# Optimization experiments

Measured on AMD Instinct MI355X. Metric: run time of the kernel, lower is better.

Reference implementation:

```python
import jax, jax.numpy as jnp
import numpy as np

B, L, D = 2, 2048, 1024
DH = 64
NH = D // DH
EPS = 1e-5
NEG = -1e30


def rms_norm(x, w):
    # x: (..., dh); norm in fp32 like the torch module, then scale by weight
    xf = x.astype(jnp.float32)
    y = xf * jax.lax.rsqrt(jnp.mean(xf * xf, axis=-1, keepdims=True) + EPS)
    return y.astype(x.dtype) * w.astype(x.dtype)


def sdpa(q, k, v, m):
    # q:(b,h,lq,dh) k,v:(b,h,lk,dh) m:(lq,lk) bool
    scale = 1.0 / jnp.sqrt(jnp.asarray(DH, q.dtype))
    s = jnp.einsum('bhqd,bhkd->bhqk', q, k) * scale
    s = jnp.where(m[None, None], s, NEG)
    p = jax.nn.softmax(s, axis=-1)
    return jnp.einsum('bhqk,bhkd->bhqd', p, v)


def setup_inputs() -> dict:
    key = jax.random.key(0)
    k1, k2, k3 = jax.random.split(key, 3)
    x = jax.random.normal(k1, (B, L, D), dtype=jnp.float32)
    mask = jnp.tril(jnp.ones((L, L), dtype=bool))  # causal: no fully-masked rows
    w_qkv = jax.random.normal(k2, (3 * D, D), dtype=jnp.float32) * (1.0 / np.sqrt(D))
    w_fc = jax.random.normal(k3, (D, D), dtype=jnp.float32) * (1.0 / np.sqrt(D))
    q_norm_w = jnp.ones((DH,), dtype=jnp.float32)
    k_norm_w = jnp.ones((DH,), dtype=jnp.float32)
    return {"x": x, "mask": mask, "w_qkv": w_qkv, "w_fc": w_fc,
            "q_norm_w": q_norm_w, "k_norm_w": k_norm_w,
            "subset_attention_size": 1024}


def reference(x, mask, w_qkv, w_fc, q_norm_w, k_norm_w, subset_attention_size):
    b, l, d = x.shape
    qkv = jnp.einsum('bld,ed->ble', x, w_qkv)  # (b,l,3d)
    q, k, v = jnp.split(qkv, 3, axis=-1)

    def heads(t):
        return t.reshape(b, l, NH, DH).transpose(0, 2, 1, 3)  # (b,nh,l,dh)

    q, k, v = heads(q), heads(k), heads(v)
    q = rms_norm(q, q_norm_w)
    k = rms_norm(k, k_norm_w)

    S = subset_attention_size
    if S is not None and S < l:
        o1 = sdpa(q[:, :, :S], k[:, :, :S], v[:, :, :S], mask[:S, :S])
        o2 = sdpa(q[:, :, S:], k, v, mask[S:, :])
        o = jnp.concatenate([o1, o2], axis=2)
    else:
        o = sdpa(q, k, v, mask)
    o = o.transpose(0, 2, 1, 3).reshape(b, l, d)  # (b,l,d)
    return jnp.einsum('bld,ed->ble', o, w_fc)
```

## Files before the change

kernel.cpp:

```cpp
#include <hip/hip_runtime.h>

typedef __bf16 bf16x8 __attribute__((ext_vector_type(8)));
typedef __bf16 bf16x4 __attribute__((ext_vector_type(4)));
typedef float f32x4 __attribute__((ext_vector_type(4)));
typedef unsigned short u16;
typedef unsigned int u32;
typedef unsigned short u16x4 __attribute__((ext_vector_type(4)));
typedef unsigned short u16x8 __attribute__((ext_vector_type(8)));

#define AS1 __attribute__((address_space(1)))
#define AS3 __attribute__((address_space(3)))

__device__ __forceinline__ u16 f2bf(float f) {
  unsigned u = __builtin_bit_cast(unsigned, f);
  u += 0x7fffu + ((u >> 16) & 1u);
  return (u16)(u >> 16);
}

__global__ __launch_bounds__(256) void cvt_all(const float* __restrict__ x,
                                               const float* __restrict__ wq,
                                               const float* __restrict__ wf,
                                               u16* __restrict__ xb, u16* __restrict__ wqb,
                                               u16* __restrict__ wfb) {
  long i = ((long)blockIdx.x * 256 + threadIdx.x) * 4;
  const float* src;
  u16* dst;
  long off;
  if (i < 4194304L) {
    src = x; dst = xb; off = i;
  } else if (i < 7340032L) {
    src = wq; dst = wqb; off = i - 4194304L;
  } else {
    src = wf; dst = wfb; off = i - 7340032L;
  }
  float4 v = *reinterpret_cast<const float4*>(src + off);
  u16x4 o;
  o.x = f2bf(v.x); o.y = f2bf(v.y); o.z = f2bf(v.z); o.w = f2bf(v.w);
  *reinterpret_cast<u16x4*>(dst + off) = o;
}

__global__ __launch_bounds__(256, 2) void gemm_qkv(const u16* __restrict__ A,
                                                   const u16* __restrict__ W,
                                                   u16* __restrict__ C,
                                                   const float* __restrict__ qw,
                                                   const float* __restrict__ kw) {
  constexpr int N = 3072, K = 1024;
  __shared__ __align__(16) u16 As[128 * 32];
  __shared__ __align__(16) u16 Bs[128 * 32];
  const int tid = threadIdx.x;
  const int lane = tid & 63;
  const int wid = tid >> 6;
  const int wm = wid >> 1, wn = wid & 1;
  const int l16 = lane & 15, g4 = lane >> 4;
  const long bm = blockIdx.x, bn = blockIdx.y;

  const int srow = tid >> 2;
  const int scol = (tid & 3) * 8;
  const u16* aA0 = A + (bm * 128 + srow) * (long)K + scol;
  const u16* aA1 = aA0 + 64 * (long)K;
  const u16* aW0 = W + (bn * 128 + srow) * (long)K + scol;
  const u16* aW1 = aW0 + 64 * (long)K;

  f32x4 acc[4][4] = {};

  for (int kt = 0; kt < K; kt += 32) {
    __builtin_amdgcn_global_load_lds((AS1 void*)(aA0 + kt), (AS3 void*)(&As[tid * 8]), 16, 0, 0);
    __builtin_amdgcn_global_load_lds((AS1 void*)(aA1 + kt), (AS3 void*)(&As[2048 + tid * 8]), 16, 0, 0);
    __builtin_amdgcn_global_load_lds((AS1 void*)(aW0 + kt), (AS3 void*)(&Bs[tid * 8]), 16, 0, 0);
    __builtin_amdgcn_global_load_lds((AS1 void*)(aW1 + kt), (AS3 void*)(&Bs[2048 + tid * 8]), 16, 0, 0);
    __syncthreads();
    bf16x8 af[4], bfr[4];
#pragma unroll
    for (int m = 0; m < 4; ++m)
      af[m] = *reinterpret_cast<const bf16x8*>(&As[(wm * 64 + m * 16 + l16) * 32 + g4 * 8]);
#pragma unroll
    for (int n = 0; n < 4; ++n)
      bfr[n] = *reinterpret_cast<const bf16x8*>(&Bs[(wn * 64 + n * 16 + l16) * 32 + g4 * 8]);
#pragma unroll
    for (int m = 0; m < 4; ++m)
#pragma unroll
      for (int n = 0; n < 4; ++n)
        acc[m][n] = __builtin_amdgcn_mfma_f32_16x16x32_bf16(af[m], bfr[n], acc[m][n], 0, 0, 0);
    __syncthreads();
  }

  if (bn < 16) {
    const float* w = (bn < 8) ? qw : kw;
    float wv[4];
#pragma unroll
    for (int n = 0; n < 4; ++n) wv[n] = w[n * 16 + l16];
#pragma unroll
    for (int m = 0; m < 4; ++m) {
#pragma unroll
      for (int j = 0; j < 4; ++j) {
        float ss = 0.f;
#pragma unroll
        for (int n = 0; n < 4; ++n) ss = fmaf(acc[m][n][j], acc[m][n][j], ss);
        ss += __shfl_xor(ss, 1);
        ss += __shfl_xor(ss, 2);
        ss += __shfl_xor(ss, 4);
        ss += __shfl_xor(ss, 8);
        const float inv = rsqrtf(ss * (1.0f / 64.0f) + 1e-5f);
#pragma unroll
        for (int n = 0; n < 4; ++n) acc[m][n][j] *= inv * wv[n];
      }
    }
  }

#pragma unroll
  for (int m = 0; m < 4; ++m)
#pragma unroll
    for (int n = 0; n < 4; ++n)
#pragma unroll
      for (int j = 0; j < 4; ++j) {
        long row = bm * 128 + wm * 64 + m * 16 + g4 * 4 + j;
        long col = bn * 128 + wn * 64 + n * 16 + l16;
        C[row * N + col] = f2bf(acc[m][n][j]);
      }
}

__global__ __launch_bounds__(256, 2) void gemm_fc(const u16* __restrict__ A,
                                                  const u16* __restrict__ W,
                                                  float* __restrict__ C) {
  constexpr int N = 1024, K = 1024;
  __shared__ __align__(16) u16 As[128 * 32];
  __shared__ __align__(16) u16 Bs[64 * 32];
  const int tid = threadIdx.x;
  const int lane = tid & 63;
  const int wid = tid >> 6;
  const int wm = wid >> 1, wn = wid & 1;
  const int l16 = lane & 15, g4 = lane >> 4;
  const long bm = blockIdx.x, bn = blockIdx.y;

  const int srow = tid >> 2;
  const int scol = (tid & 3) * 8;
  const u16* aA0 = A + (bm * 128 + srow) * (long)K + scol;
  const u16* aA1 = aA0 + 64 * (long)K;
  const u16* aW0 = W + (bn * 64 + srow) * (long)K + scol;

  f32x4 acc[4][2] = {};

  for (int kt = 0; kt < K; kt += 32) {
    __builtin_amdgcn_global_load_lds((AS1 void*)(aA0 + kt), (AS3 void*)(&As[tid * 8]), 16, 0, 0);
    __builtin_amdgcn_global_load_lds((AS1 void*)(aA1 + kt), (AS3 void*)(&As[2048 + tid * 8]), 16, 0, 0);
    __builtin_amdgcn_global_load_lds((AS1 void*)(aW0 + kt), (AS3 void*)(&Bs[tid * 8]), 16, 0, 0);
    __syncthreads();
    bf16x8 af[4], bfr[2];
#pragma unroll
    for (int m = 0; m < 4; ++m)
      af[m] = *reinterpret_cast<const bf16x8*>(&As[(wm * 64 + m * 16 + l16) * 32 + g4 * 8]);
#pragma unroll
    for (int n = 0; n < 2; ++n)
      bfr[n] = *reinterpret_cast<const bf16x8*>(&Bs[(wn * 32 + n * 16 + l16) * 32 + g4 * 8]);
#pragma unroll
    for (int m = 0; m < 4; ++m)
#pragma unroll
      for (int n = 0; n < 2; ++n)
        acc[m][n] = __builtin_amdgcn_mfma_f32_16x16x32_bf16(af[m], bfr[n], acc[m][n], 0, 0, 0);
    __syncthreads();
  }

#pragma unroll
  for (int m = 0; m < 4; ++m)
#pragma unroll
    for (int n = 0; n < 2; ++n)
#pragma unroll
      for (int j = 0; j < 4; ++j) {
        long row = bm * 128 + wm * 64 + m * 16 + g4 * 4 + j;
        long col = bn * 64 + wn * 32 + n * 16 + l16;
        C[row * N + col] = acc[m][n][j];
      }
}

__global__ __launch_bounds__(256, 4) void attn_causal(const u16* __restrict__ qkv,
                                                      u16* __restrict__ o) {
  __shared__ __align__(16) u16 Klds[2][4096];
  __shared__ __align__(16) u16 Vt[2][4096];
  __shared__ __align__(16) u16 Plds[4][640];

  const int tid = threadIdx.x, lane = tid & 63, wid = tid >> 6;
  const int l16 = lane & 15, g4 = lane >> 4;
  const int rh = wid & 1, kh = wid >> 1;

  const int f = blockIdx.x;
  const int kk = f >> 3;
  const int bh = (f & 7) * 4 + (kk >> 5);
  const int i = kk & 31;
  const int iA = i, iB = 63 - i;

  const long base = (long)(bh >> 4) * 2048 * 3072 + (bh & 15) * 64;
  const u16* qb = qkv + base;
  const u16* kb = qkv + base + 1024;
  const u16* vb = qkv + base + 2048;

  const u16* qpA = qb + ((long)iA * 32 + rh * 16 + l16) * 3072;
  const u16* qpB = qb + ((long)iB * 32 + rh * 16 + l16) * 3072;
  const bf16x8 qA0 = *reinterpret_cast<const bf16x8*>(qpA + g4 * 8);
  const bf16x8 qA1 = *reinterpret_cast<const bf16x8*>(qpA + 32 + g4 * 8);
  const bf16x8 qB0 = *reinterpret_cast<const bf16x8*>(qpB + g4 * 8);
  const bf16x8 qB1 = *reinterpret_cast<const bf16x8*>(qpB + 32 + g4 * 8);

  f32x4 accA[4] = {}, accB[4] = {};
  f32x4 laccA = {}, laccB = {};
  const float cl = 0.125f * 1.4426950408889634f;
  const float mc = -8.0f * cl;

  const int krow = tid >> 3;
  const int scolE = (((tid & 7) * 16) ^ ((krow & 7) << 4)) >> 1;
  const int vkey = (lane & 31) * 2;
  const int vd = wid * 8 + (lane >> 5) * 32;
  u16x8 vv0, vv1;

  auto stage_issue = [&](int buf, int kt) {
    __builtin_amdgcn_global_load_lds((AS1 void*)(kb + (long)(kt * 64 + krow) * 3072 + scolE),
                                     (AS3 void*)(&Klds[buf][tid * 8]), 16, 0, 0);
    __builtin_amdgcn_global_load_lds((AS1 void*)(kb + (long)(kt * 64 + krow + 32) * 3072 + scolE),
                                     (AS3 void*)(&Klds[buf][2048 + tid * 8]), 16, 0, 0);
    const u16* gv = vb + (long)(kt * 64 + vkey) * 3072 + vd;
    vv0 = *reinterpret_cast<const u16x8*>(gv);
    vv1 = *reinterpret_cast<const u16x8*>(gv + 3072);
  };
  auto vt_write = [&](int buf) {
#pragma unroll
    for (int j = 0; j < 8; ++j) {
      const int r = vd + j;
      const int boff = (vkey * 2) ^ ((r & 7) << 4);
      *reinterpret_cast<u32*>(&Vt[buf][r * 64 + (boff >> 1)]) =
          (u32)vv0[j] | ((u32)vv1[j] << 16);
    }
  };

  auto step = [&](int qt, f32x4* acc, f32x4& lacc, const bf16x8& q0, const bf16x8& q1,
                  bf16x8 (&kf)[2][2], int cur, int kt) {
    const int dd = qt - 2 * kt - kh;
    if (dd < 0) return;
    f32x4 s[2];
    __builtin_amdgcn_s_setprio(1);
#pragma unroll
    for (int kn = 0; kn < 2; ++kn) {
      f32x4 z = {0.f, 0.f, 0.f, 0.f};
      z = __builtin_amdgcn_mfma_f32_16x16x32_bf16(kf[kn][0], q0, z, 0, 0, 0);
      z = __builtin_amdgcn_mfma_f32_16x16x32_bf16(kf[kn][1], q1, z, 0, 0, 0);
      s[kn] = z;
    }
    __builtin_amdgcn_s_setprio(0);
    if (dd == 0) {
      const int qr = rh * 16 + l16;
#pragma unroll
      for (int kn = 0; kn < 2; ++kn)
#pragma unroll
        for (int j = 0; j < 4; ++j)
          if (kn * 16 + g4 * 4 + j > qr) s[kn][j] = -3e38f;
    }
#pragma unroll
    for (int kn = 0; kn < 2; ++kn) {
#pragma unroll
      for (int j = 0; j < 4; ++j) s[kn][j] = exp2f(fmaf(s[kn][j], cl, mc));
      lacc += s[kn];
    }
    u16* pl = &Plds[wid][0];
#pragma unroll
    for (int kn = 0; kn < 2; ++kn) {
      bf16x4 w4;
      w4[0] = (__bf16)s[kn][0];
      w4[1] = (__bf16)s[kn][1];
      w4[2] = (__bf16)s[kn][2];
      w4[3] = (__bf16)s[kn][3];
      *reinterpret_cast<bf16x4*>(&pl[l16 * 40 + kn * 16 + g4 * 4]) = w4;
    }
    const bf16x8 pa = *reinterpret_cast<const bf16x8*>(&pl[l16 * 40 + g4 * 8]);
    __builtin_amdgcn_s_setprio(1);
#pragma unroll
    for (int n = 0; n < 4; ++n) {
      const int rr = n * 16 + l16;
      const bf16x8 b = *reinterpret_cast<const bf16x8*>(
          &Vt[cur][rr * 64 + (((kh * 64 + g4 * 16) ^ ((rr & 7) << 4)) >> 1)]);
      acc[n] = __builtin_amdgcn_mfma_f32_16x16x32_bf16(pa, b, acc[n], 0, 0, 0);
    }
    __builtin_amdgcn_s_setprio(0);
  };

  stage_issue(0, 0);
  vt_write(0);
  __syncthreads();

  const int ktmax = (iB >> 1) + 1;
  for (int kt = 0; kt < ktmax; ++kt) {
    const int cur = kt & 1, nxt = cur ^ 1;
    const bool pre = (kt + 1 < ktmax);
    if (pre) stage_issue(nxt, kt + 1);

    bf16x8 kf[2][2];
#pragma unroll
    for (int kn = 0; kn < 2; ++kn) {
      const int row = kh * 32 + kn * 16 + l16;
#pragma unroll
      for (int ck = 0; ck < 2; ++ck)
        kf[kn][ck] = *reinterpret_cast<const bf16x8*>(
            &Klds[cur][row * 64 + (((ck * 64 + g4 * 16) ^ ((l16 & 7) << 4)) >> 1)]);
    }

    step(iA, accA, laccA, qA0, qA1, kf, cur, kt);
    step(iB, accB, laccB, qB0, qB1, kf, cur, kt);

    if (pre) vt_write(nxt);
    __syncthreads();
  }

  auto lred = [&](const f32x4& v) {
    float l = v[0] + v[1] + v[2] + v[3];
    l += __shfl_xor(l, 16);
    l += __shfl_xor(l, 32);
    return l;
  };
  float lA = lred(laccA), lB = lred(laccB);

  float* cbf = reinterpret_cast<float*>(&Klds[0][0]);
  float* lvf = reinterpret_cast<float*>(&Vt[0][0]);
  if (kh == 1) {
#pragma unroll
    for (int n = 0; n < 4; ++n) {
      *reinterpret_cast<f32x4*>(&cbf[(rh * 8 + n) * 256 + lane * 4]) = accA[n];
      *reinterpret_cast<f32x4*>(&cbf[(rh * 8 + 4 + n) * 256 + lane * 4]) = accB[n];
    }
    lvf[(rh * 2 + 0) * 64 + lane] = lA;
    lvf[(rh * 2 + 1) * 64 + lane] = lB;
  }
  __syncthreads();
  if (kh == 0) {
#pragma unroll
    for (int n = 0; n < 4; ++n) {
      accA[n] += *reinterpret_cast<const f32x4*>(&cbf[(rh * 8 + n) * 256 + lane * 4]);
      accB[n] += *reinterpret_cast<const f32x4*>(&cbf[(rh * 8 + 4 + n) * 256 + lane * 4]);
    }
    lA += lvf[(rh * 2 + 0) * 64 + lane];
    lB += lvf[(rh * 2 + 1) * 64 + lane];

    const long obase = (long)(bh >> 4) * 2048 * 1024 + (bh & 15) * 64;
    auto epi = [&](f32x4* acc, float l, int qt) {
      float lR[4];
#pragma unroll
      for (int j = 0; j < 4; ++j) lR[j] = __shfl(l, g4 * 4 + j, 16);
      u16* op = o + obase + ((long)qt * 32 + rh * 16 + g4 * 4) * 1024;
#pragma unroll
      for (int n = 0; n < 4; ++n)
#pragma unroll
        for (int j = 0; j < 4; ++j)
          op[j * 1024 + n * 16 + l16] = f2bf(acc[n][j] / lR[j]);
    };
    epi(accA, lA, iA);
    epi(accB, lB, iB);
  }
}

extern "C" void kernel_launch(void* const* d_in, const int* in_sizes, int n_in,
                              void* d_out, int out_size, void* d_ws, size_t ws_size,
                              hipStream_t stream) {
  const float* x = (const float*)d_in[0];
  const float* w_qkv = (const float*)d_in[2];
  const float* w_fc = (const float*)d_in[3];
  const float* qw = (const float*)d_in[4];
  const float* kw = (const float*)d_in[5];
  float* out = (float*)d_out;

  char* ws = (char*)d_ws;
  u16* xb    = (u16*)(ws);
  u16* wqkvb = (u16*)(ws + (8L << 20));
  u16* wfcb  = (u16*)(ws + (14L << 20));
  u16* qkv   = (u16*)(ws + (16L << 20));
  u16* ob    = (u16*)(ws + (40L << 20));

  cvt_all<<<8192, 256, 0, stream>>>(x, w_qkv, w_fc, xb, wqkvb, wfcb);
  gemm_qkv<<<dim3(32, 24), 256, 0, stream>>>(xb, wqkvb, qkv, qw, kw);
  attn_causal<<<1024, 256, 0, stream>>>(qkv, ob);
  gemm_fc<<<dim3(32, 16), 256, 0, stream>>>(ob, wfcb, out);
}
```

Measured before the change: 115.7 us.

## Pre-transpose V in a separate kernel and enlarge attention query tiles

Adds a vtrans kernel that writes V transposed per head into the free x-bf16 workspace, so the attention kernel can stage V with async global_load_lds instead of register loads followed by a scattered LDS transpose. The attention kernel now gives each block 64-row query tiles (paired causal tiles i and 31-i), with each wave owning 16 query rows across all 64 keys. This removes the cross-wave key-half reduction in the epilogue and halves the grid. It costs an extra kernel launch and an extra pass over V in memory, and lowers the occupancy hint from 4 to 2 blocks per CU.

```diff
diff --git a/kernel.cpp b/kernel.cpp
--- a/kernel.cpp
+++ b/kernel.cpp
@@ -172,29 +172,52 @@
       }
 }
 
-__global__ __launch_bounds__(256, 4) void attn_causal(const u16* __restrict__ qkv,
+__global__ __launch_bounds__(256) void vtrans(const u16* __restrict__ qkv,
+                                              u16* __restrict__ vt) {
+  __shared__ u16 T[64][66];
+  const int tid = threadIdx.x;
+  const int f = blockIdx.x;
+  const int bh = (f & 7) * 4 + (f >> 8);
+  const int ktile = (f >> 3) & 31;
+  const long vbase = (long)(bh >> 4) * 2048 * 3072 + (bh & 15) * 64 + 2048;
+  const int r = tid >> 2, c = (tid & 3) * 16;
+  const u16* src = qkv + vbase + (long)(ktile * 64 + r) * 3072 + c;
+  *reinterpret_cast<u16x8*>(&T[r][c]) = *reinterpret_cast<const u16x8*>(src);
+  *reinterpret_cast<u16x8*>(&T[r][c + 8]) = *reinterpret_cast<const u16x8*>(src + 8);
+  __syncthreads();
+  const int dr = tid >> 2, kc = (tid & 3) * 16;
+  u16 buf[16];
+#pragma unroll
+  for (int j = 0; j < 16; ++j) buf[j] = T[kc + j][dr];
+  u16* dst = vt + (long)bh * 131072 + (long)dr * 2048 + ktile * 64 + kc;
+  *reinterpret_cast<u16x8*>(dst) = *reinterpret_cast<u16x8*>(&buf[0]);
+  *reinterpret_cast<u16x8*>(dst + 8) = *reinterpret_cast<u16x8*>(&buf[8]);
+}
+
+__global__ __launch_bounds__(256, 2) void attn_causal(const u16* __restrict__ qkv,
+                                                      const u16* __restrict__ vt,
                                                       u16* __restrict__ o) {
   __shared__ __align__(16) u16 Klds[2][4096];
-  __shared__ __align__(16) u16 Vt[2][4096];
-  __shared__ __align__(16) u16 Plds[4][640];
+  __shared__ __align__(16) u16 Vlds[2][4096];
+  __shared__ __align__(16) u16 Plds[4][1024];
 
   const int tid = threadIdx.x, lane = tid & 63, wid = tid >> 6;
   const int l16 = lane & 15, g4 = lane >> 4;
-  const int rh = wid & 1, kh = wid >> 1;
+  const int h8 = (l16 & 7) << 4;
 
   const int f = blockIdx.x;
-  const int kk = f >> 3;
-  const int bh = (f & 7) * 4 + (kk >> 5);
-  const int i = kk & 31;
-  const int iA = i, iB = 63 - i;
+  const int g = f >> 3;
+  const int bh = (f & 7) * 4 + (g >> 4);
+  const int i = g & 15;
+  const int iA = i, iB = 31 - i;
 
   const long base = (long)(bh >> 4) * 2048 * 3072 + (bh & 15) * 64;
   const u16* qb = qkv + base;
   const u16* kb = qkv + base + 1024;
-  const u16* vb = qkv + base + 2048;
-
-  const u16* qpA = qb + ((long)iA * 32 + rh * 16 + l16) * 3072;
-  const u16* qpB = qb + ((long)iB * 32 + rh * 16 + l16) * 3072;
+  const u16* vtb = vt + (long)bh * 131072;
+
+  const u16* qpA = qb + ((long)iA * 64 + wid * 16 + l16) * 3072;
+  const u16* qpB = qb + ((long)iB * 64 + wid * 16 + l16) * 3072;
   const bf16x8 qA0 = *reinterpret_cast<const bf16x8*>(qpA + g4 * 8);
   const bf16x8 qA1 = *reinterpret_cast<const bf16x8*>(qpA + 32 + g4 * 8);
   const bf16x8 qB0 = *reinterpret_cast<const bf16x8*>(qpB + g4 * 8);
@@ -207,150 +230,109 @@
 
   const int krow = tid >> 3;
   const int scolE = (((tid & 7) * 16) ^ ((krow & 7) << 4)) >> 1;
-  const int vkey = (lane & 31) * 2;
-  const int vd = wid * 8 + (lane >> 5) * 32;
-  u16x8 vv0, vv1;
 
   auto stage_issue = [&](int buf, int kt) {
     __builtin_amdgcn_global_load_lds((AS1 void*)(kb + (long)(kt * 64 + krow) * 3072 + scolE),
                                      (AS3 void*)(&Klds[buf][tid * 8]), 16, 0, 0);
     __builtin_amdgcn_global_load_lds((AS1 void*)(kb + (long)(kt * 64 + krow + 32) * 3072 + scolE),
                                      (AS3 void*)(&Klds[buf][2048 + tid * 8]), 16, 0, 0);
-    const u16* gv = vb + (long)(kt * 64 + vkey) * 3072 + vd;
-    vv0 = *reinterpret_cast<const u16x8*>(gv);
-    vv1 = *reinterpret_cast<const u16x8*>(gv + 3072);
+    __builtin_amdgcn_global_load_lds((AS1 void*)(vtb + (long)krow * 2048 + kt * 64 + scolE),
+                                     (AS3 void*)(&Vlds[buf][tid * 8]), 16, 0, 0);
+    __builtin_amdgcn_global_load_lds((AS1 void*)(vtb + (long)(krow + 32) * 2048 + kt * 64 + scolE),
+                                     (AS3 void*)(&Vlds[buf][2048 + tid * 8]), 16, 0, 0);
   };
-  auto vt_write = [&](int buf) {
-#pragma unroll
-    for (int j = 0; j < 8; ++j) {
-      const int r = vd + j;
-      const int boff = (vkey * 2) ^ ((r & 7) << 4);
-      *reinterpret_cast<u32*>(&Vt[buf][r * 64 + (boff >> 1)]) =
-          (u32)vv0[j] | ((u32)vv1[j] << 16);
-    }
-  };
-
-  auto step = [&](int qt, f32x4* acc, f32x4& lacc, const bf16x8& q0, const bf16x8& q1,
-                  bf16x8 (&kf)[2][2], int cur, int kt) {
-    const int dd = qt - 2 * kt - kh;
-    if (dd < 0) return;
-    f32x4 s[2];
+
+  auto tile_step = [&](f32x4* acc, f32x4& lacc, const bf16x8& q0, const bf16x8& q1, bool diag,
+                       bf16x8 (&kf)[4][2], bf16x8 (&vf)[4][2]) {
+    f32x4 s[4];
     __builtin_amdgcn_s_setprio(1);
 #pragma unroll
-    for (int kn = 0; kn < 2; ++kn) {
+    for (int kn = 0; kn < 4; ++kn) {
       f32x4 z = {0.f, 0.f, 0.f, 0.f};
       z = __builtin_amdgcn_mfma_f32_16x16x32_bf16(kf[kn][0], q0, z, 0, 0, 0);
       z = __builtin_amdgcn_mfma_f32_16x16x32_bf16(kf[kn][1], q1, z, 0, 0, 0);
       s[kn] = z;
     }
     __builtin_amdgcn_s_setprio(0);
-    if (dd == 0) {
-      const int qr = rh * 16 + l16;
-#pragma unroll
-      for (int kn = 0; kn < 2; ++kn)
+    if (diag) {
+      const int qrel = wid * 16 + l16;
+#pragma unroll
+      for (int kn = 0; kn < 4; ++kn)
 #pragma unroll
         for (int j = 0; j < 4; ++j)
-          if (kn * 16 + g4 * 4 + j > qr) s[kn][j] = -3e38f;
-    }
-#pragma unroll
-    for (int kn = 0; kn < 2; ++kn) {
+          if (kn * 16 + g4 * 4 + j > qrel) s[kn][j] = -3e38f;
+    }
+#pragma unroll
+    for (int kn = 0; kn < 4; ++kn) {
 #pragma unroll
       for (int j = 0; j < 4; ++j) s[kn][j] = exp2f(fmaf(s[kn][j], cl, mc));
       lacc += s[kn];
     }
     u16* pl = &Plds[wid][0];
 #pragma unroll
-    for (int kn = 0; kn < 2; ++kn) {
+    for (int kn = 0; kn < 4; ++kn) {
       bf16x4 w4;
       w4[0] = (__bf16)s[kn][0];
       w4[1] = (__bf16)s[kn][1];
       w4[2] = (__bf16)s[kn][2];
       w4[3] = (__bf16)s[kn][3];
-      *reinterpret_cast<bf16x4*>(&pl[l16 * 40 + kn * 16 + g4 * 4]) = w4;
-    }
-    const bf16x8 pa = *reinterpret_cast<const bf16x8*>(&pl[l16 * 40 + g4 * 8]);
+      const int boff = (kn * 32 + g4 * 8) ^ h8;
+      *reinterpret_cast<bf16x4*>(&pl[l16 * 64 + (boff >> 1)]) = w4;
+    }
+    const bf16x8 pa0 = *reinterpret_cast<const bf16x8*>(&pl[l16 * 64 + (((g4 * 16) ^ h8) >> 1)]);
+    const bf16x8 pa1 =
+        *reinterpret_cast<const bf16x8*>(&pl[l16 * 64 + (((64 + g4 * 16) ^ h8) >> 1)]);
     __builtin_amdgcn_s_setprio(1);
 #pragma unroll
     for (int n = 0; n < 4; ++n) {
-      const int rr = n * 16 + l16;
-      const bf16x8 b = *reinterpret_cast<const bf16x8*>(
-          &Vt[cur][rr * 64 + (((kh * 64 + g4 * 16) ^ ((rr & 7) << 4)) >> 1)]);
-      acc[n] = __builtin_amdgcn_mfma_f32_16x16x32_bf16(pa, b, acc[n], 0, 0, 0);
+      acc[n] = __builtin_amdgcn_mfma_f32_16x16x32_bf16(pa0, vf[n][0], acc[n], 0, 0, 0);
+      acc[n] = __builtin_amdgcn_mfma_f32_16x16x32_bf16(pa1, vf[n][1], acc[n], 0, 0, 0);
     }
     __builtin_amdgcn_s_setprio(0);
   };
 
   stage_issue(0, 0);
-  vt_write(0);
   __syncthreads();
 
-  const int ktmax = (iB >> 1) + 1;
-  for (int kt = 0; kt < ktmax; ++kt) {
+  for (int kt = 0; kt <= iB; ++kt) {
     const int cur = kt & 1, nxt = cur ^ 1;
-    const bool pre = (kt + 1 < ktmax);
-    if (pre) stage_issue(nxt, kt + 1);
-
-    bf16x8 kf[2][2];
-#pragma unroll
-    for (int kn = 0; kn < 2; ++kn) {
-      const int row = kh * 32 + kn * 16 + l16;
-#pragma unroll
-      for (int ck = 0; ck < 2; ++ck)
-        kf[kn][ck] = *reinterpret_cast<const bf16x8*>(
-            &Klds[cur][row * 64 + (((ck * 64 + g4 * 16) ^ ((l16 & 7) << 4)) >> 1)]);
-    }
-
-    step(iA, accA, laccA, qA0, qA1, kf, cur, kt);
-    step(iB, accB, laccB, qB0, qB1, kf, cur, kt);
-
-    if (pre) vt_write(nxt);
-    __syncthreads();
-  }
-
-  auto lred = [&](const f32x4& v) {
-    float l = v[0] + v[1] + v[2] + v[3];
+    if (kt < iB) stage_issue(nxt, kt + 1);
+
+    bf16x8 kf[4][2], vf[4][2];
+#pragma unroll
+    for (int kn = 0; kn < 4; ++kn) {
+      const int row = kn * 16 + l16;
+#pragma unroll
+      for (int ck = 0; ck < 2; ++ck) {
+        const int boff = (ck * 64 + g4 * 16) ^ h8;
+        kf[kn][ck] = *reinterpret_cast<const bf16x8*>(&Klds[cur][row * 64 + (boff >> 1)]);
+        vf[kn][ck] = *reinterpret_cast<const bf16x8*>(&Vlds[cur][row * 64 + (boff >> 1)]);
+      }
+    }
+
+    if (kt <= iA) tile_step(accA, laccA, qA0, qA1, kt == iA, kf, vf);
+    tile_step(accB, laccB, qB0, qB1, kt == iB, kf, vf);
+
+    __syncthreads();
+  }
+
+  const long obase = (long)(bh >> 4) * 2048 * 1024 + (bh & 15) * 64;
+  auto epi = [&](f32x4* acc, const f32x4& lacc, int qt) {
+    float l = lacc[0] + lacc[1] + lacc[2] + lacc[3];
     l += __shfl_xor(l, 16);
     l += __shfl_xor(l, 32);
-    return l;
+    float lR[4];
+#pragma unroll
+    for (int j = 0; j < 4; ++j) lR[j] = __shfl(l, g4 * 4 + j, 16);
+    u16* op = o + obase + ((long)qt * 64 + wid * 16 + g4 * 4) * 1024;
+#pragma unroll
+    for (int n = 0; n < 4; ++n)
+#pragma unroll
+      for (int j = 0; j < 4; ++j)
+        op[j * 1024 + n * 16 + l16] = f2bf(acc[n][j] / lR[j]);
   };
-  float lA = lred(laccA), lB = lred(laccB);
-
-  float* cbf = reinterpret_cast<float*>(&Klds[0][0]);
-  float* lvf = reinterpret_cast<float*>(&Vt[0][0]);
-  if (kh == 1) {
-#pragma unroll
-    for (int n = 0; n < 4; ++n) {
-      *reinterpret_cast<f32x4*>(&cbf[(rh * 8 + n) * 256 + lane * 4]) = accA[n];
-      *reinterpret_cast<f32x4*>(&cbf[(rh * 8 + 4 + n) * 256 + lane * 4]) = accB[n];
-    }
-    lvf[(rh * 2 + 0) * 64 + lane] = lA;
-    lvf[(rh * 2 + 1) * 64 + lane] = lB;
-  }
-  __syncthreads();
-  if (kh == 0) {
-#pragma unroll
-    for (int n = 0; n < 4; ++n) {
-      accA[n] += *reinterpret_cast<const f32x4*>(&cbf[(rh * 8 + n) * 256 + lane * 4]);
-      accB[n] += *reinterpret_cast<const f32x4*>(&cbf[(rh * 8 + 4 + n) * 256 + lane * 4]);
-    }
-    lA += lvf[(rh * 2 + 0) * 64 + lane];
-    lB += lvf[(rh * 2 + 1) * 64 + lane];
-
-    const long obase = (long)(bh >> 4) * 2048 * 1024 + (bh & 15) * 64;
-    auto epi = [&](f32x4* acc, float l, int qt) {
-      float lR[4];
-#pragma unroll
-      for (int j = 0; j < 4; ++j) lR[j] = __shfl(l, g4 * 4 + j, 16);
-      u16* op = o + obase + ((long)qt * 32 + rh * 16 + g4 * 4) * 1024;
-#pragma unroll
-      for (int n = 0; n < 4; ++n)
-#pragma unroll
-        for (int j = 0; j < 4; ++j)
-          op[j * 1024 + n * 16 + l16] = f2bf(acc[n][j] / lR[j]);
-    };
-    epi(accA, lA, iA);
-    epi(accB, lB, iB);
-  }
+  epi(accA, laccA, iA);
+  epi(accB, laccB, iB);
 }
 
 extern "C" void kernel_launch(void* const* d_in, const int* in_sizes, int n_in,
@@ -369,9 +351,11 @@
   u16* wfcb  = (u16*)(ws + (14L << 20));
   u16* qkv   = (u16*)(ws + (16L << 20));
   u16* ob    = (u16*)(ws + (40L << 20));
+  u16* vt    = xb;
 
   cvt_all<<<8192, 256, 0, stream>>>(x, w_qkv, w_fc, xb, wqkvb, wfcb);
   gemm_qkv<<<dim3(32, 24), 256, 0, stream>>>(xb, wqkvb, qkv, qw, kw);
-  attn_causal<<<1024, 256, 0, stream>>>(qkv, ob);
+  vtrans<<<1024, 256, 0, stream>>>(qkv, vt);
+  attn_causal<<<512, 256, 0, stream>>>(qkv, vt, ob);
   gemm_fc<<<dim3(32, 16), 256, 0, stream>>>(ob, wfcb, out);
 }
```

New measurement: 113.5 us. Within noise of the previous version (-2.0%).
